# Kernel optimization log

Hardware: AMD Instinct MI355X
Metric: run time of the kernel (lower is better)

The kernel has to match this reference:

```python
import jax, jax.numpy as jnp
import numpy as np
from jax import lax

WINDOW_SIZE = 11
SIGMA = 1.5
DATA_RANGE = 1.0


def _gaussian_window(channels):
    coords = jnp.arange(WINDOW_SIZE, dtype=jnp.float32) - WINDOW_SIZE // 2
    g = jnp.exp(-coords ** 2 / (2.0 * SIGMA ** 2))
    g = g / g.sum()
    w2d = jnp.outer(g, g)
    w2d = w2d / w2d.sum()
    # depthwise kernel: (C, 1, K, K) in OIHW with feature_group_count=C
    return jnp.broadcast_to(w2d, (channels, 1, WINDOW_SIZE, WINDOW_SIZE))


def _dwconv(x, window, channels):
    pad = WINDOW_SIZE // 2
    return lax.conv_general_dilated(
        x, window,
        window_strides=(1, 1),
        padding=[(pad, pad), (pad, pad)],
        dimension_numbers=('NCHW', 'OIHW', 'NCHW'),
        feature_group_count=channels,
    )


def setup_inputs() -> dict:
    key = jax.random.key(0)
    k1, k2 = jax.random.split(key)
    B, C, H, W = 16, 3, 512, 512
    x = jax.random.uniform(k1, (B, C, H, W), dtype=jnp.float32)
    y = jax.random.uniform(k2, (B, C, H, W), dtype=jnp.float32)
    return {"x": x, "y": y}


def reference(x, y):
    channels = x.shape[1]
    window = _gaussian_window(channels)
    mu_x = _dwconv(x, window, channels)
    mu_y = _dwconv(y, window, channels)
    mu_x2 = mu_x * mu_x
    mu_y2 = mu_y * mu_y
    mu_xy = mu_x * mu_y
    sigma_x2 = _dwconv(x * x, window, channels) - mu_x2
    sigma_y2 = _dwconv(y * y, window, channels) - mu_y2
    sigma_xy = _dwconv(x * y, window, channels) - mu_xy
    c1 = (0.01 * DATA_RANGE) ** 2
    c2 = (0.03 * DATA_RANGE) ** 2
    ssim_map = (2 * mu_xy + c1) * (2 * sigma_xy + c2) / (
        (mu_x2 + mu_y2 + c1) * (sigma_x2 + sigma_y2 + c2) + 1e-08)
    per_image = ssim_map.mean(axis=(1, 2, 3))
    return 1.0 - per_image.mean()
```

## Files before the change

### kernel.cpp

```cpp
#include <hip/hip_runtime.h>
#include <math.h>


#define IMG_W 512
#define IMG_H 512
#define PLANES 48
#define TX 64
#define TY 32
#define RAD 5
#define NT 256
#define GDX (IMG_W / TX)
#define GDY (IMG_H / TY)
#define NBLK (GDX * GDY * PLANES)

#define SROWS 48
#define SCH   20
#define SSTR  88
#define HSTR  56
#define GC    (1.f / (2.f * 1.5f * 1.5f))

typedef _Float16 h2 __attribute__((ext_vector_type(2)));
typedef _Float16 h4 __attribute__((ext_vector_type(4)));
typedef _Float16 h8 __attribute__((ext_vector_type(8)));
typedef float f32x4 __attribute__((ext_vector_type(4)));

__device__ __forceinline__ h2 pkrtz(float a, float b) {
    auto t = __builtin_amdgcn_cvt_pkrtz(a, b);
    h2 r;
    __builtin_memcpy(&r, &t, sizeof(r));
    return r;
}

__device__ __forceinline__ h4 pack4(f32x4 a) {
    const h2 lo = pkrtz(a[0], a[1]), hi = pkrtz(a[2], a[3]);
    h4 v;
    v[0] = lo.x; v[1] = lo.y; v[2] = hi.x; v[3] = hi.y;
    return v;
}

__global__ __launch_bounds__(NT, 3) void ssim_tile_kernel(
    const float* __restrict__ x, const float* __restrict__ y,
    float* __restrict__ partials)
{
    __shared__ __align__(16) _Float16 sIn[SROWS * SSTR];
    __shared__ __align__(16) _Float16 dIn[SROWS * SSTR];
    __shared__ __align__(16) _Float16 Ht[4 * TX * HSTR];
    __shared__ float wave_sums[NT / 64];

    const int tid = threadIdx.x;
    const int l   = tid & 63, wid = tid >> 6;
    const int q   = l >> 4,  fc  = l & 15;

    float inv, cv;
    {
        float s = 0.f;
        #pragma unroll
        for (int k = 0; k < 11; ++k) {
            const float d = (float)(k - RAD);
            s += expf(-d * d * GC);
        }
        inv = 1.f / s;
        float s2 = 0.f;
        #pragma unroll
        for (int k = 0; k < 11; ++k) {
            const float d = (float)(k - RAD);
            s2 += (float)(_Float16)(expf(-d * d * GC) * inv);
        }
        cv = 1.f / (s2 * s2);
    }

    h8 whB, wvA;
    #pragma unroll
    for (int e = 0; e < 8; ++e) {
        const int t  = 8 * q + e;
        const int k1 = t - fc - 3;
        const int k2 = t - fc;
        float g1 = 0.f, g2 = 0.f;
        if (k1 >= 0 && k1 <= 10) {
            const float d = (float)(k1 - RAD);
            g1 = expf(-d * d * GC) * inv;
        }
        if (k2 >= 0 && k2 <= 10) {
            const float d = (float)(k2 - RAD);
            g2 = expf(-d * d * GC) * inv;
        }
        whB[e] = (_Float16)g1;
        wvA[e] = (_Float16)g2;
    }

    const int plane = blockIdx.z;
    const float* __restrict__ xp = x + (size_t)plane * IMG_H * IMG_W;
    const float* __restrict__ yp = y + (size_t)plane * IMG_H * IMG_W;
    const int C0 = blockIdx.x * TX;
    const int R0 = blockIdx.y * TY;

    for (int it = tid; it < SROWS * SCH; it += NT) {
        const int i  = it / SCH;
        const int c  = it - i * SCH;
        const int gr = R0 - RAD + i;
        const int gc = C0 - 8 + 4 * c;
        float4 xa = make_float4(0.f, 0.f, 0.f, 0.f);
        float4 ya = make_float4(0.f, 0.f, 0.f, 0.f);
        if ((unsigned)gr < (unsigned)IMG_H && (unsigned)gc < (unsigned)IMG_W) {
            xa = *(const float4*)(xp + (size_t)gr * IMG_W + gc);
            ya = *(const float4*)(yp + (size_t)gr * IMG_W + gc);
        }
        const h2 x01 = pkrtz(xa.x, xa.y), x23 = pkrtz(xa.z, xa.w);
        const h2 y01 = pkrtz(ya.x, ya.y), y23 = pkrtz(ya.z, ya.w);
        const h2 s01 = x01 + y01, s23 = x23 + y23;
        const h2 d01 = x01 - y01, d23 = x23 - y23;
        h4 sv, dv;
        sv[0] = s01.x; sv[1] = s01.y; sv[2] = s23.x; sv[3] = s23.y;
        dv[0] = d01.x; dv[1] = d01.y; dv[2] = d23.x; dv[3] = d23.y;
        *(h4*)&sIn[i * SSTR + 4 * c] = sv;
        *(h4*)&dIn[i * SSTR + 4 * c] = dv;
    }
    __syncthreads();

    const int c0 = 16 * wid;
    const f32x4 zz = {0.f, 0.f, 0.f, 0.f};
    #pragma unroll
    for (int i0 = 0; i0 < SROWS; i0 += 16) {
        const int aoff = (i0 + fc) * SSTR + c0 + 8 * q;
        const h8 sA = *(const h8*)&sIn[aoff];
        const h8 dA = *(const h8*)&dIn[aoff];
        const h8 s2A = sA * sA;
        const h8 d2A = dA * dA;
        const f32x4 hS  = __builtin_amdgcn_mfma_f32_16x16x32_f16(sA,  whB, zz, 0, 0, 0);
        const f32x4 hD  = __builtin_amdgcn_mfma_f32_16x16x32_f16(dA,  whB, zz, 0, 0, 0);
        const f32x4 hS2 = __builtin_amdgcn_mfma_f32_16x16x32_f16(s2A, whB, zz, 0, 0, 0);
        const f32x4 hD2 = __builtin_amdgcn_mfma_f32_16x16x32_f16(d2A, whB, zz, 0, 0, 0);
        const int hoff = (c0 + fc) * HSTR + i0 + 4 * q;
        *(h4*)&Ht[0 * TX * HSTR + hoff] = pack4(hS);
        *(h4*)&Ht[1 * TX * HSTR + hoff] = pack4(hD);
        *(h4*)&Ht[2 * TX * HSTR + hoff] = pack4(hS2);
        *(h4*)&Ht[3 * TX * HSTR + hoff] = pack4(hD2);
    }
    __syncthreads();

    float local = 0.f;
    #pragma unroll
    for (int m = 0; m < TY / 16; ++m) {
        const int boff = (c0 + fc) * HSTR + 16 * m + 8 * q;
        const f32x4 aS  = __builtin_amdgcn_mfma_f32_16x16x32_f16(
            wvA, *(const h8*)&Ht[0 * TX * HSTR + boff], zz, 0, 0, 0);
        const f32x4 aD  = __builtin_amdgcn_mfma_f32_16x16x32_f16(
            wvA, *(const h8*)&Ht[1 * TX * HSTR + boff], zz, 0, 0, 0);
        const f32x4 aS2 = __builtin_amdgcn_mfma_f32_16x16x32_f16(
            wvA, *(const h8*)&Ht[2 * TX * HSTR + boff], zz, 0, 0, 0);
        const f32x4 aD2 = __builtin_amdgcn_mfma_f32_16x16x32_f16(
            wvA, *(const h8*)&Ht[3 * TX * HSTR + boff], zz, 0, 0, 0);
        #pragma unroll
        for (int r = 0; r < 4; ++r) {
            const float mS = aS[r]  * cv, mD = aD[r]  * cv;
            const float eS = aS2[r] * cv, eD = aD2[r] * cv;
            const float ms2 = mS * mS, md2 = mD * mD;
            const float Pm = 0.5f * (ms2 - md2);
            const float Qm = 0.5f * (ms2 + md2);
            const float Pe = 0.5f * (eS - eD);
            const float Qe = 0.5f * (eS + eD);
            const float c1 = 1e-4f, c2 = 9e-4f;
            const float num = (Pm + c1) * (Pe - Pm + c2);
            const float den = (Qm + c1) * (Qe - Qm + c2) + 1e-8f;
            local += num * __builtin_amdgcn_rcpf(den);
        }
    }

    #pragma unroll
    for (int off = 32; off > 0; off >>= 1)
        local += __shfl_down(local, off, 64);
    if (l == 0) wave_sums[wid] = local;
    __syncthreads();
    if (tid == 0) {
        const float s = wave_sums[0] + wave_sums[1] + wave_sums[2] + wave_sums[3];
        const int bid = blockIdx.x + GDX * (blockIdx.y + GDY * blockIdx.z);
        partials[bid] = s;
    }
}

__global__ __launch_bounds__(NT) void ssim_finalize_kernel(
    const float* __restrict__ partials, float* __restrict__ out)
{
    const int tid = threadIdx.x;
    double s = 0.0;
    #pragma unroll 4
    for (int i = tid; i < NBLK; i += NT) s += (double)partials[i];
    #pragma unroll
    for (int off = 32; off > 0; off >>= 1)
        s += __shfl_down(s, off, 64);
    __shared__ double ws_[NT / 64];
    const int lane = tid & 63, wv = tid >> 6;
    if (lane == 0) ws_[wv] = s;
    __syncthreads();
    if (tid == 0) {
        const double t = ws_[0] + ws_[1] + ws_[2] + ws_[3];
        const double n = (double)PLANES * IMG_H * IMG_W;
        out[0] = (float)(1.0 - t / n);
    }
}

extern "C" void kernel_launch(void* const* d_in, const int* in_sizes, int n_in,
                              void* d_out, int out_size, void* d_ws, size_t ws_size,
                              hipStream_t stream)
{
    const float* x = (const float*)d_in[0];
    const float* y = (const float*)d_in[1];
    float* out = (float*)d_out;
    float* partials = (float*)d_ws;

    dim3 grid(GDX, GDY, PLANES);
    ssim_tile_kernel<<<grid, NT, 0, stream>>>(x, y, partials);
    ssim_finalize_kernel<<<1, NT, 0, stream>>>(partials, out);
}
```

Baseline: 148.5 us.

## Load conv operands directly from global memory, dropping LDS input staging

Each lane now loads its sum/difference MFMA operands straight from global memory into registers, instead of first staging fp16 tiles in shared memory behind a block barrier. A template splits interior and border tiles so interior tiles skip bounds checks. Shared memory now holds only the horizontal-pass buffer, which lets occupancy rise to 5 blocks per CU. The barrier between passes is removed because each wave reads back only its own columns, and the Gaussian weights are computed with a cheaper exp2 builtin. The cost is that overlapping halo rows are re-fetched from global memory or cache rather than shared across the block.

```diff
diff --git a/kernel.cpp b/kernel.cpp
--- a/kernel.cpp
+++ b/kernel.cpp
@@ -14,15 +14,28 @@
 #define NBLK (GDX * GDY * PLANES)
 
 #define SROWS 48
-#define SCH   20
-#define SSTR  88
 #define HSTR  56
-#define GC    (1.f / (2.f * 1.5f * 1.5f))
+#define INVW  0.26601181f
+#define GC2   0.32059890f
 
 typedef _Float16 h2 __attribute__((ext_vector_type(2)));
 typedef _Float16 h4 __attribute__((ext_vector_type(4)));
 typedef _Float16 h8 __attribute__((ext_vector_type(8)));
 typedef float f32x4 __attribute__((ext_vector_type(4)));
+
+__device__ __forceinline__ float exp2_fast(float a) {
+#if __has_builtin(__builtin_amdgcn_exp2f)
+    return __builtin_amdgcn_exp2f(a);
+#else
+    return exp2f(a);
+#endif
+}
+
+__device__ __forceinline__ float wbandf(int idx) {
+    const float fd = (float)(idx - 5);
+    const float g = exp2_fast(-(fd * fd) * GC2) * INVW;
+    return ((unsigned)idx <= 10u) ? g : 0.f;
+}
 
 __device__ __forceinline__ h2 pkrtz(float a, float b) {
     auto t = __builtin_amdgcn_cvt_pkrtz(a, b);
@@ -38,92 +51,48 @@
     return v;
 }
 
-__global__ __launch_bounds__(NT, 3) void ssim_tile_kernel(
-    const float* __restrict__ x, const float* __restrict__ y,
-    float* __restrict__ partials)
-{
-    __shared__ __align__(16) _Float16 sIn[SROWS * SSTR];
-    __shared__ __align__(16) _Float16 dIn[SROWS * SSTR];
-    __shared__ __align__(16) _Float16 Ht[4 * TX * HSTR];
-    __shared__ float wave_sums[NT / 64];
-
-    const int tid = threadIdx.x;
-    const int l   = tid & 63, wid = tid >> 6;
-    const int q   = l >> 4,  fc  = l & 15;
-
-    float inv, cv;
-    {
-        float s = 0.f;
-        #pragma unroll
-        for (int k = 0; k < 11; ++k) {
-            const float d = (float)(k - RAD);
-            s += expf(-d * d * GC);
+template<bool INTERIOR>
+__device__ __forceinline__ void load_sd(const float* __restrict__ xp,
+                                        const float* __restrict__ yp,
+                                        int gr, int gc, h8& sA, h8& dA)
+{
+    const float4 z4 = make_float4(0.f, 0.f, 0.f, 0.f);
+    float4 xa = z4, xb = z4, ya = z4, yb = z4;
+    if (INTERIOR || (unsigned)gr < (unsigned)IMG_H) {
+        const float* rx = xp + (size_t)gr * IMG_W;
+        const float* ry = yp + (size_t)gr * IMG_W;
+        if (INTERIOR || (unsigned)gc < (unsigned)IMG_W) {
+            xa = *(const float4*)(rx + gc);
+            ya = *(const float4*)(ry + gc);
         }
-        inv = 1.f / s;
-        float s2 = 0.f;
-        #pragma unroll
-        for (int k = 0; k < 11; ++k) {
-            const float d = (float)(k - RAD);
-            s2 += (float)(_Float16)(expf(-d * d * GC) * inv);
+        if (INTERIOR || (unsigned)(gc + 4) < (unsigned)IMG_W) {
+            xb = *(const float4*)(rx + gc + 4);
+            yb = *(const float4*)(ry + gc + 4);
         }
-        cv = 1.f / (s2 * s2);
-    }
-
-    h8 whB, wvA;
-    #pragma unroll
-    for (int e = 0; e < 8; ++e) {
-        const int t  = 8 * q + e;
-        const int k1 = t - fc - 3;
-        const int k2 = t - fc;
-        float g1 = 0.f, g2 = 0.f;
-        if (k1 >= 0 && k1 <= 10) {
-            const float d = (float)(k1 - RAD);
-            g1 = expf(-d * d * GC) * inv;
-        }
-        if (k2 >= 0 && k2 <= 10) {
-            const float d = (float)(k2 - RAD);
-            g2 = expf(-d * d * GC) * inv;
-        }
-        whB[e] = (_Float16)g1;
-        wvA[e] = (_Float16)g2;
-    }
-
-    const int plane = blockIdx.z;
-    const float* __restrict__ xp = x + (size_t)plane * IMG_H * IMG_W;
-    const float* __restrict__ yp = y + (size_t)plane * IMG_H * IMG_W;
-    const int C0 = blockIdx.x * TX;
-    const int R0 = blockIdx.y * TY;
-
-    for (int it = tid; it < SROWS * SCH; it += NT) {
-        const int i  = it / SCH;
-        const int c  = it - i * SCH;
-        const int gr = R0 - RAD + i;
-        const int gc = C0 - 8 + 4 * c;
-        float4 xa = make_float4(0.f, 0.f, 0.f, 0.f);
-        float4 ya = make_float4(0.f, 0.f, 0.f, 0.f);
-        if ((unsigned)gr < (unsigned)IMG_H && (unsigned)gc < (unsigned)IMG_W) {
-            xa = *(const float4*)(xp + (size_t)gr * IMG_W + gc);
-            ya = *(const float4*)(yp + (size_t)gr * IMG_W + gc);
-        }
-        const h2 x01 = pkrtz(xa.x, xa.y), x23 = pkrtz(xa.z, xa.w);
-        const h2 y01 = pkrtz(ya.x, ya.y), y23 = pkrtz(ya.z, ya.w);
-        const h2 s01 = x01 + y01, s23 = x23 + y23;
-        const h2 d01 = x01 - y01, d23 = x23 - y23;
-        h4 sv, dv;
-        sv[0] = s01.x; sv[1] = s01.y; sv[2] = s23.x; sv[3] = s23.y;
-        dv[0] = d01.x; dv[1] = d01.y; dv[2] = d23.x; dv[3] = d23.y;
-        *(h4*)&sIn[i * SSTR + 4 * c] = sv;
-        *(h4*)&dIn[i * SSTR + 4 * c] = dv;
-    }
-    __syncthreads();
-
-    const int c0 = 16 * wid;
+    }
+    const h2 xh0 = pkrtz(xa.x, xa.y), xh1 = pkrtz(xa.z, xa.w);
+    const h2 xh2 = pkrtz(xb.x, xb.y), xh3 = pkrtz(xb.z, xb.w);
+    const h2 yh0 = pkrtz(ya.x, ya.y), yh1 = pkrtz(ya.z, ya.w);
+    const h2 yh2 = pkrtz(yb.x, yb.y), yh3 = pkrtz(yb.z, yb.w);
+    const h2 s0 = xh0 + yh0, s1 = xh1 + yh1, s2 = xh2 + yh2, s3 = xh3 + yh3;
+    const h2 d0 = xh0 - yh0, d1 = xh1 - yh1, d2 = xh2 - yh2, d3 = xh3 - yh3;
+    sA[0] = s0.x; sA[1] = s0.y; sA[2] = s1.x; sA[3] = s1.y;
+    sA[4] = s2.x; sA[5] = s2.y; sA[6] = s3.x; sA[7] = s3.y;
+    dA[0] = d0.x; dA[1] = d0.y; dA[2] = d1.x; dA[3] = d1.y;
+    dA[4] = d2.x; dA[5] = d2.y; dA[6] = d3.x; dA[7] = d3.y;
+}
+
+template<bool INTERIOR>
+__device__ __forceinline__ void hconv_all(
+    const float* __restrict__ xp, const float* __restrict__ yp,
+    int R0, int gcol, int fc, int q, int c0, h8 whB,
+    _Float16* __restrict__ Ht)
+{
     const f32x4 zz = {0.f, 0.f, 0.f, 0.f};
     #pragma unroll
     for (int i0 = 0; i0 < SROWS; i0 += 16) {
-        const int aoff = (i0 + fc) * SSTR + c0 + 8 * q;
-        const h8 sA = *(const h8*)&sIn[aoff];
-        const h8 dA = *(const h8*)&dIn[aoff];
+        h8 sA, dA;
+        load_sd<INTERIOR>(xp, yp, R0 - RAD + i0 + fc, gcol, sA, dA);
         const h8 s2A = sA * sA;
         const h8 d2A = dA * dA;
         const f32x4 hS  = __builtin_amdgcn_mfma_f32_16x16x32_f16(sA,  whB, zz, 0, 0, 0);
@@ -136,8 +105,49 @@
         *(h4*)&Ht[2 * TX * HSTR + hoff] = pack4(hS2);
         *(h4*)&Ht[3 * TX * HSTR + hoff] = pack4(hD2);
     }
-    __syncthreads();
-
+}
+
+__global__ __launch_bounds__(NT, 5) void ssim_tile_kernel(
+    const float* __restrict__ x, const float* __restrict__ y,
+    float* __restrict__ partials)
+{
+    __shared__ __align__(16) _Float16 Ht[4 * TX * HSTR];
+    __shared__ float wave_sums[NT / 64];
+
+    const int tid = threadIdx.x;
+    const int l   = tid & 63, wid = tid >> 6;
+    const int q   = l >> 4,  fc  = l & 15;
+
+    float s2w = 0.f;
+    #pragma unroll
+    for (int k = 0; k <= 10; ++k) s2w += (float)(_Float16)wbandf(k);
+    const float cv = 1.f / (s2w * s2w);
+
+    h8 whB, wvA;
+    #pragma unroll
+    for (int e = 0; e < 8; ++e) whB[e] = (_Float16)wbandf(8 * q + e - fc - 3);
+    #pragma unroll
+    for (int e = 0; e < 5; ++e) wvA[e] = whB[e + 3];
+    #pragma unroll
+    for (int e = 5; e < 8; ++e) wvA[e] = (_Float16)wbandf(8 * q + e - fc);
+
+    const int plane = blockIdx.z;
+    const float* __restrict__ xp = x + (size_t)plane * IMG_H * IMG_W;
+    const float* __restrict__ yp = y + (size_t)plane * IMG_H * IMG_W;
+    const int C0 = blockIdx.x * TX;
+    const int R0 = blockIdx.y * TY;
+    const int c0 = 16 * wid;
+    const int gcol = C0 + c0 - 8 + 8 * q;
+
+    const bool interior =
+        (blockIdx.x >= 1) && (blockIdx.x <= GDX - 2) &&
+        (blockIdx.y >= 1) && (blockIdx.y <= GDY - 2);
+
+    if (interior) hconv_all<true >(xp, yp, R0, gcol, fc, q, c0, whB, Ht);
+    else          hconv_all<false>(xp, yp, R0, gcol, fc, q, c0, whB, Ht);
+
+
+    const f32x4 zz = {0.f, 0.f, 0.f, 0.f};
     float local = 0.f;
     #pragma unroll
     for (int m = 0; m < TY / 16; ++m) {
```

Result: faster. 137.5 us (-7.4%).
